# Kernel optimization log

Measured on AMD Instinct MI355X. Metric: run time of the kernel, lower is better.

Reference implementation:

```python
import jax, jax.numpy as jnp
import numpy as np
import math

D_MODEL = 2048
N_HEADS = 16
D_HEAD = D_MODEL // N_HEADS
SCALE = 1.0 / math.sqrt(D_HEAD)


def setup_inputs() -> dict:
    key = jax.random.key(0)
    kx, kq, kk, kv, ko = jax.random.split(key, 5)
    x = jax.random.normal(kx, (2, 2048, D_MODEL), dtype=jnp.float32)
    W_q = jax.random.normal(kq, (D_MODEL, D_MODEL), dtype=jnp.float32)
    W_k = jax.random.normal(kk, (D_MODEL, D_MODEL), dtype=jnp.float32)
    W_v = jax.random.normal(kv, (D_MODEL, D_MODEL), dtype=jnp.float32) * math.sqrt(2.0 / D_MODEL)
    W_o = jax.random.normal(ko, (D_MODEL, D_MODEL), dtype=jnp.float32) * math.sqrt(2.0 / D_MODEL)
    return {"x": x, "W_q": W_q, "W_k": W_k, "W_v": W_v, "W_o": W_o}


def reference(x, W_q, W_k, W_v, W_o) -> jnp.ndarray:
    B, S, D = x.shape
    q = (x @ W_q).reshape(B, S, N_HEADS, D_HEAD)  # [b, q, h, dh]
    k = (x @ W_k).reshape(B, S, N_HEADS, D_HEAD)  # [b, k, h, dh]
    v = x @ W_v                                    # [b, k, d_model] (NOT split into heads)
    scores = jnp.einsum('bqhd,bkhd->bhqk', q, k)   # [b, h, q, k]
    # Faithful quirk: additive -1e9 causal mask applied BEFORE the scale.
    mask = jnp.triu(jnp.full((S, S), -1e9, dtype=scores.dtype), k=1)
    scores = (scores + mask) * SCALE
    probs = jax.nn.softmax(scores, axis=-1)
    # Faithful quirk: sums over heads h AND keys k against full-width v.
    out = jnp.einsum('bhqk,bkd->bqd', probs, v)    # [b, q, d_model]
    return out @ W_o
```

## Files before the change

### kernel.cpp

```cpp
#include <hip/hip_runtime.h>

typedef unsigned short u16;
typedef __attribute__((ext_vector_type(8))) short bf16x8;
typedef __attribute__((ext_vector_type(4))) float f32x4;

#define DEV __device__ __forceinline__
#define EXP2(x) __builtin_amdgcn_exp2f(x)
#define LOG2(x) __builtin_amdgcn_logf(x)

DEV u16 f2bf(float f) {
  union { float f; unsigned u; } v; v.f = f;
  unsigned r = v.u + 0x7fffu + ((v.u >> 16) & 1u);
  return (u16)(r >> 16);
}
DEV float bf2f(u16 h) {
  union { unsigned u; float f; } v; v.u = ((unsigned)h) << 16;
  return v.f;
}
DEV f32x4 mfma16(bf16x8 a, bf16x8 b, f32x4 c) {
  return __builtin_amdgcn_mfma_f32_16x16x32_bf16(a, b, c, 0, 0, 0);
}
DEV void cp16(const u16* g, u16* l) {
  __builtin_amdgcn_global_load_lds((__attribute__((address_space(1))) void*)g,
                                   (__attribute__((address_space(3))) void*)l, 16, 0, 0);
}

__global__ __launch_bounds__(256) void split_pair(const float4* __restrict__ x,
                                                  u16* __restrict__ hi, u16* __restrict__ lo) {
  const size_t i = (size_t)blockIdx.x * 256 + threadIdx.x;
  const float4 v = x[i];
  ushort4 h, l;
  h.x = f2bf(v.x); l.x = f2bf(v.x - bf2f(h.x));
  h.y = f2bf(v.y); l.y = f2bf(v.y - bf2f(h.y));
  h.z = f2bf(v.z); l.z = f2bf(v.z - bf2f(h.z));
  h.w = f2bf(v.w); l.w = f2bf(v.w - bf2f(h.w));
  *(ushort4*)&hi[i * 4] = h;
  *(ushort4*)&lo[i * 4] = l;
}

template<bool LO>
__global__ __launch_bounds__(256) void transpose_split(const float* __restrict__ W,
                                                       u16* __restrict__ Th, u16* __restrict__ Tl) {
  __shared__ float t[64][65];
  const int r0 = blockIdx.y * 64, c0 = blockIdx.x * 64;
  const int rr = threadIdx.x >> 4, c4 = (threadIdx.x & 15) * 4;
#pragma unroll
  for (int p = 0; p < 4; ++p) {
    const float4 v = *(const float4*)&W[(size_t)(r0 + p * 16 + rr) * 2048 + c0 + c4];
    t[p * 16 + rr][c4 + 0] = v.x; t[p * 16 + rr][c4 + 1] = v.y;
    t[p * 16 + rr][c4 + 2] = v.z; t[p * 16 + rr][c4 + 3] = v.w;
  }
  __syncthreads();
#pragma unroll
  for (int p = 0; p < 4; ++p) {
    const int cc = p * 16 + rr;
    const float v0 = t[c4 + 0][cc], v1 = t[c4 + 1][cc], v2 = t[c4 + 2][cc], v3 = t[c4 + 3][cc];
    ushort4 h;
    h.x = f2bf(v0); h.y = f2bf(v1); h.z = f2bf(v2); h.w = f2bf(v3);
    *(ushort4*)&Th[(size_t)(c0 + cc) * 2048 + r0 + c4] = h;
    if constexpr (LO) {
      ushort4 l;
      l.x = f2bf(v0 - bf2f(h.x)); l.y = f2bf(v1 - bf2f(h.y));
      l.z = f2bf(v2 - bf2f(h.z)); l.w = f2bf(v3 - bf2f(h.w));
      *(ushort4*)&Tl[(size_t)(c0 + cc) * 2048 + r0 + c4] = l;
    }
  }
}

__global__ __launch_bounds__(256, 2) void gemm_qk(
    const u16* __restrict__ Aph, const u16* __restrict__ Apl,
    const u16* __restrict__ Bqh, const u16* __restrict__ Bql,
    const u16* __restrict__ Bkh, const u16* __restrict__ Bkl,
    u16* __restrict__ Qh, u16* __restrict__ Ql,
    u16* __restrict__ Kh, u16* __restrict__ Kl) {
  extern __shared__ u16 lds[];
  char* ldsb = (char*)lds;
  const int tid = threadIdx.x;
  const int wave = tid >> 6, lane = tid & 63;
  const int li = lane & 15, l4 = lane >> 4;
  const int lin0 = ((int)blockIdx.y << 4) | (int)blockIdx.x;
  const int xcd = lin0 & 7, idx = lin0 >> 3;
  const int m0 = ((xcd << 2) | (idx & 3)) * 128;
  const int n0 = (idx >> 2) * 128;
  const int wr = (wave >> 1) * 64, wc = (wave & 1) * 64;

  const f32x4 fz = {0.f, 0.f, 0.f, 0.f};
  f32x4 accQ[4][4], accK[4][4];
#pragma unroll
  for (int m = 0; m < 4; ++m)
#pragma unroll
    for (int n = 0; n < 4; ++n) { accQ[m][n] = fz; accK[m][n] = fz; }

  const int o = tid * 16;
  const int op = o ^ (((o >> 7) & 7) << 4);
  const int srow = op >> 6, scol = (op & 63) >> 1;
  const size_t aoff = (size_t)(m0 + srow) * 2048 + scol;
  const size_t boff = (size_t)(n0 + srow) * 2048 + scol;
  const size_t rstep = (size_t)64 * 2048;
  const int s0 = tid * 8, s1 = 2048 + tid * 8;

  const int arow = wr + li, brow = wc + li;
  const int rsA = (arow * 64 + l4 * 16) ^ (((arow >> 1) & 7) << 4);
  const int rsB = (brow * 64 + l4 * 16) ^ (((brow >> 1) & 7) << 4);

#pragma unroll 1
  for (int k0 = 0; k0 < 2048; k0 += 32) {
    cp16(Aph + aoff + k0,         &lds[s0]);
    cp16(Aph + aoff + rstep + k0, &lds[s1]);
    cp16(Apl + aoff + k0,         &lds[4096 + s0]);
    cp16(Apl + aoff + rstep + k0, &lds[4096 + s1]);
    cp16(Bqh + boff + k0,         &lds[8192 + s0]);
    cp16(Bqh + boff + rstep + k0, &lds[8192 + s1]);
    cp16(Bql + boff + k0,         &lds[12288 + s0]);
    cp16(Bql + boff + rstep + k0, &lds[12288 + s1]);
    cp16(Bkh + boff + k0,         &lds[16384 + s0]);
    cp16(Bkh + boff + rstep + k0, &lds[16384 + s1]);
    cp16(Bkl + boff + k0,         &lds[20480 + s0]);
    cp16(Bkl + boff + rstep + k0, &lds[20480 + s1]);
    __syncthreads();
    bf16x8 af[4], alf[4];
#pragma unroll
    for (int m = 0; m < 4; ++m) {
      af[m]  = *(const bf16x8*)(ldsb + rsA + m * 1024);
      alf[m] = *(const bf16x8*)(ldsb + 8192 + rsA + m * 1024);
    }
    {
      bf16x8 bh[4], bl[4];
#pragma unroll
      for (int n = 0; n < 4; ++n) {
        bh[n] = *(const bf16x8*)(ldsb + 16384 + rsB + n * 1024);
        bl[n] = *(const bf16x8*)(ldsb + 24576 + rsB + n * 1024);
      }
#pragma unroll
      for (int m = 0; m < 4; ++m)
#pragma unroll
        for (int n = 0; n < 4; ++n) {
          accQ[m][n] = mfma16(af[m], bh[n], accQ[m][n]);
          accQ[m][n] = mfma16(af[m], bl[n], accQ[m][n]);
          accQ[m][n] = mfma16(alf[m], bh[n], accQ[m][n]);
        }
    }
    {
      bf16x8 bh[4], bl[4];
#pragma unroll
      for (int n = 0; n < 4; ++n) {
        bh[n] = *(const bf16x8*)(ldsb + 32768 + rsB + n * 1024);
        bl[n] = *(const bf16x8*)(ldsb + 40960 + rsB + n * 1024);
      }
#pragma unroll
      for (int m = 0; m < 4; ++m)
#pragma unroll
        for (int n = 0; n < 4; ++n) {
          accK[m][n] = mfma16(af[m], bh[n], accK[m][n]);
          accK[m][n] = mfma16(af[m], bl[n], accK[m][n]);
          accK[m][n] = mfma16(alf[m], bh[n], accK[m][n]);
        }
    }
    __syncthreads();
  }

#pragma unroll
  for (int m = 0; m < 4; ++m) {
#pragma unroll
    for (int n = 0; n < 4; ++n) {
      const int rg0 = m0 + wr + m * 16 + l4 * 4;
      const int cg  = n0 + wc + n * 16 + li;
#pragma unroll
      for (int r = 0; r < 4; ++r) {
        const float vq = accQ[m][n][r];
        const u16 hq = f2bf(vq);
        Qh[(size_t)(rg0 + r) * 2048 + cg] = hq;
        Ql[(size_t)(rg0 + r) * 2048 + cg] = f2bf(vq - bf2f(hq));
        const float vk = accK[m][n][r];
        const u16 hk = f2bf(vk);
        Kh[(size_t)(rg0 + r) * 2048 + cg] = hk;
        Kl[(size_t)(rg0 + r) * 2048 + cg] = f2bf(vk - bf2f(hk));
      }
    }
  }
}

template<int OUTMODE, bool KLIM>
__global__ __launch_bounds__(256, 2) void gemm_bt(
    const u16* __restrict__ Aph, const u16* __restrict__ Bph,
    void* __restrict__ C0,
    const int M, const int N, const int K, const int bShift) {
  extern __shared__ u16 lds[];
  constexpr int T_BH = 4096;
  const int tid = threadIdx.x;
  const int wave = tid >> 6, lane = tid & 63;
  const int li = lane & 15, l4 = lane >> 4;
  const int lin0 = ((int)blockIdx.y << 4) | (int)blockIdx.x;
  const int xcd = lin0 & 7, idx = lin0 >> 3;
  const int m0 = ((xcd << 2) | (idx & 3)) * 128;
  const int n0 = (idx >> 2) * 128;
  const int wr = (wave >> 1) * 64, wc = (wave & 1) * 64;
  const u16* Bh = Bph;
  if (bShift) { const size_t s = (size_t)(m0 >> 11) * (size_t)bShift; Bh += s; }

  const f32x4 fz = {0.f, 0.f, 0.f, 0.f};
  f32x4 acc[4][4];
#pragma unroll
  for (int m = 0; m < 4; ++m)
#pragma unroll
    for (int n = 0; n < 4; ++n) acc[m][n] = fz;

  const size_t aoff = (size_t)(m0 + (tid >> 2)) * K + (tid & 3) * 8;
  const size_t boff = (size_t)(n0 + (tid >> 2)) * K + (tid & 3) * 8;
  const size_t rstep = (size_t)64 * K;
  const int s0 = tid * 8, s1 = 2048 + tid * 8;
  const int abase = (wr + li) * 32 + l4 * 8;
  const int bbase = (wc + li) * 32 + l4 * 8;
  const int kEnd = KLIM ? ((m0 & 2047) + 128 < K ? (m0 & 2047) + 128 : K) : K;

#pragma unroll 1
  for (int k0 = 0; k0 < kEnd; k0 += 32) {
    cp16(Aph + aoff + k0,         &lds[s0]);
    cp16(Aph + aoff + rstep + k0, &lds[s1]);
    cp16(Bh + boff + k0,          &lds[T_BH + s0]);
    cp16(Bh + boff + rstep + k0,  &lds[T_BH + s1]);
    __syncthreads();
    bf16x8 af[4], bf_[4];
#pragma unroll
    for (int m = 0; m < 4; ++m) af[m] = *(const bf16x8*)&lds[abase + m * 512];
#pragma unroll
    for (int n = 0; n < 4; ++n) bf_[n] = *(const bf16x8*)&lds[T_BH + bbase + n * 512];
#pragma unroll
    for (int m = 0; m < 4; ++m)
#pragma unroll
      for (int n = 0; n < 4; ++n)
        acc[m][n] = mfma16(af[m], bf_[n], acc[m][n]);
    __syncthreads();
  }

#pragma unroll
  for (int m = 0; m < 4; ++m) {
#pragma unroll
    for (int n = 0; n < 4; ++n) {
      const int rg0 = m0 + wr + m * 16 + l4 * 4;
      const int cg  = n0 + wc + n * 16 + li;
      if constexpr (OUTMODE == 1) {
        u16* Cs = (u16*)C0;
#pragma unroll
        for (int r = 0; r < 4; ++r) Cs[(size_t)(rg0 + r) * N + cg] = f2bf(acc[m][n][r]);
      } else if constexpr (OUTMODE == 2) {
        u16* Vt = (u16*)C0;
        ushort4 pk;
        pk.x = f2bf(acc[m][n][0]); pk.y = f2bf(acc[m][n][1]);
        pk.z = f2bf(acc[m][n][2]); pk.w = f2bf(acc[m][n][3]);
        *(ushort4*)&Vt[(size_t)(rg0 >> 11) * 4194304 + (size_t)cg * 2048 + (rg0 & 2047)] = pk;
      } else {
        float* Cf = (float*)C0;
#pragma unroll
        for (int r = 0; r < 4; ++r) Cf[(size_t)(rg0 + r) * N + cg] = acc[m][n][r];
      }
    }
  }
}

#define C2EXP 0.1275174381027786f

__global__ __launch_bounds__(256) void attn_lse_part(
    const u16* __restrict__ Qh, const u16* __restrict__ Ql,
    const u16* __restrict__ Kh, const u16* __restrict__ Kl,
    float* __restrict__ Mp, float* __restrict__ Lp) {
  const int j = blockIdx.x, qt = 15 - (int)blockIdx.y, hb = blockIdx.z;
  const int b = hb >> 4, h = hb & 15;
  const int tid = threadIdx.x;
  const int nch = (qt >> 2) + 1;
  if (j >= nch) {
    if (tid < 128) {
      const size_t o = ((size_t)hb * 4 + j) * 2048 + qt * 128 + tid;
      Mp[o] = -3.0e38f; Lp[o] = 0.f;
    }
    return;
  }
  __shared__ __align__(16) u16 kb[16384];
  const int wave = tid >> 6, lane = tid & 63;
  const int li = lane & 15, l4 = lane >> 4;
  const int q0w = qt * 128 + wave * 32;
  const int rs = ((li << 6) | (l4 << 4)) ^ (((li >> 1) & 7) << 4);

  bf16x8 qfh[2][4], qfl[2][4];
#pragma unroll
  for (int mf = 0; mf < 2; ++mf) {
    const size_t qo = ((size_t)(b * 2048 + q0w + mf * 16 + li)) * 2048 + h * 128 + l4 * 8;
#pragma unroll
    for (int ks = 0; ks < 4; ++ks) {
      qfh[mf][ks] = *(const bf16x8*)&Qh[qo + ks * 32];
      qfl[mf][ks] = *(const bf16x8*)&Ql[qo + ks * 32];
    }
  }
  float m[2][4], l[2][4];
#pragma unroll
  for (int mf = 0; mf < 2; ++mf)
#pragma unroll
    for (int r = 0; r < 4; ++r) { m[mf][r] = -3.0e38f; l[mf][r] = 0.f; }

  const int kst = j * 8;
  const int ken = min(j * 8 + 8, qt * 2 + 2);
  const size_t kgbase = ((size_t)b * 2048) * 2048 + h * 128;
  const f32x4 fz = {0.f, 0.f, 0.f, 0.f};

#pragma unroll 1
  for (int t = kst; t < ken; ++t) {
    __syncthreads();
#pragma unroll
    for (int i = 0; i < 4; ++i) {
      const int o = (tid + i * 256) * 16;
      const int op = o ^ (((o >> 7) & 7) << 4);
      const int dck = op >> 12, s = (op >> 6) & 63, dl = (op >> 1) & 31;
      const size_t g = kgbase + (size_t)(t * 64 + s) * 2048 + dck * 32 + dl;
      cp16(Kh + g, kb + (o >> 1));
      cp16(Kl + g, kb + 8192 + (o >> 1));
    }
    __syncthreads();
#pragma unroll
    for (int sn = 0; sn < 4; ++sn) {
      if (64 * t + 16 * sn <= q0w + 31) {
        f32x4 a0 = fz, a1 = fz;
        __builtin_amdgcn_s_setprio(1);
#pragma unroll
        for (int ks = 0; ks < 4; ++ks) {
          const bf16x8 kh = *(const bf16x8*)((const char*)kb + ks * 4096 + (sn << 10) + rs);
          const bf16x8 kl = *(const bf16x8*)((const char*)kb + 16384 + ks * 4096 + (sn << 10) + rs);
          a0 = mfma16(qfh[0][ks], kh, a0);
          a0 = mfma16(qfh[0][ks], kl, a0);
          a0 = mfma16(qfl[0][ks], kh, a0);
          a1 = mfma16(qfh[1][ks], kh, a1);
          a1 = mfma16(qfh[1][ks], kl, a1);
          a1 = mfma16(qfl[1][ks], kh, a1);
        }
        __builtin_amdgcn_s_setprio(0);
        const int kg = t * 64 + sn * 16 + li;
#pragma unroll
        for (int r = 0; r < 4; ++r) {
          {
            const float aa = (kg <= q0w + l4 * 4 + r) ? a0[r] : -3.3e38f;
            if (__all(aa <= m[0][r])) {
              l[0][r] += EXP2((aa - m[0][r]) * C2EXP);
            } else {
              const float mn = fmaxf(m[0][r], aa);
              l[0][r] = l[0][r] * EXP2((m[0][r] - mn) * C2EXP) + EXP2((aa - mn) * C2EXP);
              m[0][r] = mn;
            }
          }
          {
            const float aa = (kg <= q0w + 16 + l4 * 4 + r) ? a1[r] : -3.3e38f;
            if (__all(aa <= m[1][r])) {
              l[1][r] += EXP2((aa - m[1][r]) * C2EXP);
            } else {
              const float mn = fmaxf(m[1][r], aa);
              l[1][r] = l[1][r] * EXP2((m[1][r] - mn) * C2EXP) + EXP2((aa - mn) * C2EXP);
              m[1][r] = mn;
            }
          }
        }
      }
    }
  }
#pragma unroll
  for (int off = 1; off <= 8; off <<= 1) {
#pragma unroll
    for (int mf = 0; mf < 2; ++mf)
#pragma unroll
      for (int r = 0; r < 4; ++r) {
        const float om = __shfl_xor(m[mf][r], off, 64);
        const float ol = __shfl_xor(l[mf][r], off, 64);
        const float mn = fmaxf(m[mf][r], om);
        l[mf][r] = l[mf][r] * EXP2((m[mf][r] - mn) * C2EXP) + ol * EXP2((om - mn) * C2EXP);
        m[mf][r] = mn;
      }
  }
  if (li == 0) {
#pragma unroll
    for (int mf = 0; mf < 2; ++mf)
#pragma unroll
      for (int r = 0; r < 4; ++r) {
        const size_t o = ((size_t)hb * 4 + j) * 2048 + q0w + mf * 16 + l4 * 4 + r;
        Mp[o] = m[mf][r];
        Lp[o] = l[mf][r];
      }
  }
}

__global__ __launch_bounds__(256) void attn_lse_merge(
    const float* __restrict__ Mp, const float* __restrict__ Lp, float* __restrict__ LSE) {
  const int id = blockIdx.x * 256 + threadIdx.x;
  const int q = id & 2047, hb = id >> 11;
  const size_t base = (size_t)hb * 4 * 2048 + q;
  float m = Mp[base], l = Lp[base];
#pragma unroll
  for (int jj = 1; jj < 4; ++jj) {
    const float om = Mp[base + jj * 2048];
    const float ol = Lp[base + jj * 2048];
    const float mn = fmaxf(m, om);
    l = l * EXP2((m - mn) * C2EXP) + ol * EXP2((om - mn) * C2EXP);
    m = mn;
  }
  LSE[(size_t)hb * 2048 + q] = m * C2EXP + LOG2(l);
}

__global__ __launch_bounds__(256) void attn_psum(
    const u16* __restrict__ Qh, const u16* __restrict__ Ql,
    const u16* __restrict__ Kh, const u16* __restrict__ Kl,
    const float* __restrict__ LSE, u16* __restrict__ Psum) {
  const int kt = blockIdx.x, qt = blockIdx.y, b = blockIdx.z;
  const int q0 = qt * 128, k0 = kt * 128;
  const int tid = threadIdx.x;

  if (kt > qt) {
    const size_t o = ((size_t)(b * 2048 + q0 + (tid >> 1))) * 2048 + k0 + (tid & 1) * 64;
    const uint4 z = {0u, 0u, 0u, 0u};
#pragma unroll
    for (int j2 = 0; j2 < 8; ++j2) *(uint4*)&Psum[o + j2 * 8] = z;
    return;
  }

  extern __shared__ u16 kb2[];
  const int wave = tid >> 6, lane = tid & 63;
  const int li = lane & 15, l4 = lane >> 4;
  const int q0w = q0 + wave * 32;
  const int rs = ((li << 6) | (l4 << 4)) ^ (((li >> 1) & 7) << 4);
  const int snmax = (kt == qt) ? (wave * 2 + 2) : 8;

  const f32x4 fz = {0.f, 0.f, 0.f, 0.f};
  f32x4 ps[2][8];
#pragma unroll
  for (int mf = 0; mf < 2; ++mf)
#pragma unroll
    for (int sn = 0; sn < 8; ++sn) ps[mf][sn] = fz;

  const size_t kgbase = ((size_t)(b * 2048 + k0)) * 2048;
  const size_t qbase0 = ((size_t)(b * 2048 + q0w + li)) * 2048 + l4 * 8;
  const size_t qbase1 = qbase0 + (size_t)16 * 2048;
  const size_t lbase  = (size_t)(b * 16) * 2048 + q0w + l4 * 4;

#pragma unroll 1
  for (int h = 0; h < 16; ++h) {
    __syncthreads();
#pragma unroll
    for (int i = 0; i < 8; ++i) {
      const int o = (tid + i * 256) * 16;
      const int op = o ^ (((o >> 7) & 7) << 4);
      const int dck = op >> 13, s = (op >> 6) & 127, dl = (op >> 1) & 31;
      const size_t g = kgbase + (size_t)s * 2048 + h * 128 + dck * 32 + dl;
      cp16(Kh + g, kb2 + (o >> 1));
      cp16(Kl + g, kb2 + 16384 + (o >> 1));
    }
    bf16x8 qfh0[4], qfl0[4], qfh1[4], qfl1[4];
    float clse[2][4];
#pragma unroll
    for (int ks = 0; ks < 4; ++ks) {
      qfh0[ks] = *(const bf16x8*)&Qh[qbase0 + (size_t)h * 128 + ks * 32];
      qfl0[ks] = *(const bf16x8*)&Ql[qbase0 + (size_t)h * 128 + ks * 32];
      qfh1[ks] = *(const bf16x8*)&Qh[qbase1 + (size_t)h * 128 + ks * 32];
      qfl1[ks] = *(const bf16x8*)&Ql[qbase1 + (size_t)h * 128 + ks * 32];
    }
#pragma unroll
    for (int mf = 0; mf < 2; ++mf)
#pragma unroll
      for (int r = 0; r < 4; ++r)
        clse[mf][r] = LSE[lbase + (size_t)h * 2048 + mf * 16 + r];
    __syncthreads();

#pragma unroll
    for (int sn = 0; sn < 8; ++sn) {
      if (sn < snmax) {
        f32x4 a0 = fz, a1 = fz;
        __builtin_amdgcn_s_setprio(1);
#pragma unroll
        for (int ks = 0; ks < 4; ++ks) {
          const bf16x8 kh = *(const bf16x8*)((const char*)kb2 + ks * 8192 + (sn << 10) + rs);
          const bf16x8 kl = *(const bf16x8*)((const char*)kb2 + 32768 + ks * 8192 + (sn << 10) + rs);
          a0 = mfma16(qfh0[ks], kh, a0);
          a0 = mfma16(qfh0[ks], kl, a0);
          a0 = mfma16(qfl0[ks], kh, a0);
          a1 = mfma16(qfh1[ks], kh, a1);
          a1 = mfma16(qfh1[ks], kl, a1);
          a1 = mfma16(qfl1[ks], kh, a1);
        }
        __builtin_amdgcn_s_setprio(0);
        const int kg = k0 + sn * 16 + li;
#pragma unroll
        for (int r = 0; r < 4; ++r) {
          if (kg <= q0w + l4 * 4 + r)      ps[0][sn][r] += EXP2(a0[r] * C2EXP - clse[0][r]);
          if (kg <= q0w + 16 + l4 * 4 + r) ps[1][sn][r] += EXP2(a1[r] * C2EXP - clse[1][r]);
        }
      }
    }
  }

#pragma unroll
  for (int mf = 0; mf < 2; ++mf)
#pragma unroll
    for (int sn = 0; sn < 8; ++sn) {
      const size_t o0 = ((size_t)(b * 2048 + q0w + mf * 16 + l4 * 4)) * 2048 + k0 + sn * 16 + li;
#pragma unroll
      for (int r = 0; r < 4; ++r) Psum[o0 + (size_t)r * 2048] = f2bf(ps[mf][sn][r]);
    }
}

extern "C" void kernel_launch(void* const* d_in, const int* in_sizes, int n_in,
                              void* d_out, int out_size, void* d_ws, size_t ws_size,
                              hipStream_t stream) {
  (void)in_sizes; (void)n_in; (void)out_size; (void)ws_size;
  const float* x  = (const float*)d_in[0];
  const float* Wq = (const float*)d_in[1];
  const float* Wk = (const float*)d_in[2];
  const float* Wv = (const float*)d_in[3];
  const float* Wo = (const float*)d_in[4];
  u16* ws = (u16*)d_ws;
  const size_t E8 = 8388608, E4 = 4194304;
  u16* xh = ws;
  u16* xl = ws + E8;
  u16* Qh = ws + 2 * E8;
  u16* Ql = ws + 3 * E8;
  u16* Kh = ws + 4 * E8;
  u16* Kl = ws + 5 * E8;
  u16* Vt = ws + 6 * E8;
  u16* WTh = ws + 7 * E8;
  u16* WTl = ws + 7 * E8 + E4;
  u16* WTb = ws + 7 * E8 + 2 * E4;
  u16* WkTh = Vt;
  u16* WkTl = Vt + E4;
  float* LSEf = (float*)WTl;
  float* Mp   = LSEf + 65536;
  float* Lp   = Mp + 262144;
  u16* Psum = xl;
  u16* out1 = xh;

  split_pair<<<8192, 256, 0, stream>>>((const float4*)x, xh, xl);

  dim3 tg(32, 32);

  transpose_split<true ><<<tg, 256, 0, stream>>>(Wq, WTh, WTl);
  transpose_split<true ><<<tg, 256, 0, stream>>>(Wk, WkTh, WkTl);
  transpose_split<false><<<tg, 256, 0, stream>>>(Wv, WTb, nullptr);

  gemm_qk<<<dim3(16, 32), 256, 49152, stream>>>(
      xh, xl, WTh, WTl, WkTh, WkTl, Qh, Ql, Kh, Kl);

  gemm_bt<2, false><<<dim3(16, 32), 256, 16384, stream>>>(
      xh, WTb, Vt, 4096, 2048, 2048, 0);

  attn_lse_part<<<dim3(4, 16, 32), 256, 0, stream>>>(Qh, Ql, Kh, Kl, Mp, Lp);
  attn_lse_merge<<<256, 256, 0, stream>>>(Mp, Lp, LSEf);
  attn_psum<<<dim3(16, 16, 2), 256, 65536, stream>>>(Qh, Ql, Kh, Kl, LSEf, Psum);

  gemm_bt<1, true><<<dim3(16, 32), 256, 16384, stream>>>(
      Psum, Vt, out1, 4096, 2048, 2048, 4194304);

  transpose_split<false><<<tg, 256, 0, stream>>>(Wo, WTb, nullptr);
  gemm_bt<3, false><<<dim3(16, 32), 256, 16384, stream>>>(
      out1, WTb, d_out, 4096, 2048, 2048, 0);
}
```

Baseline: 565.5 us.

## Halve attn_psum key tile, split MFMA accumulators, merge weight transposes

Shrinks the attn_psum key tile from 128 to 64, doubling the grid. It uses 32KB of static LDS instead of 64KB dynamic, to raise occupancy and trim causal waste on the diagonal. The hi/lo compensated MFMA chain now uses independent accumulators to break the serial dependency. The three weight transposes are fused into one launch to cut launch overhead. In exchange, Q fragments and LSE values are reloaded twice as often across key tiles.

Result: slower. 616.0 us (+8.9%).

```diff
diff --git a/kernel.cpp b/kernel.cpp
--- a/kernel.cpp
+++ b/kernel.cpp
@@ -36,6 +36,40 @@
   h.w = f2bf(v.w); l.w = f2bf(v.w - bf2f(h.w));
   *(ushort4*)&hi[i * 4] = h;
   *(ushort4*)&lo[i * 4] = l;
+}
+
+__global__ __launch_bounds__(256) void transpose_all(
+    const float* __restrict__ Wq, const float* __restrict__ Wk, const float* __restrict__ Wv,
+    u16* __restrict__ qTh, u16* __restrict__ qTl,
+    u16* __restrict__ kTh, u16* __restrict__ kTl, u16* __restrict__ vTh) {
+  const float* W; u16* Th; u16* Tl; bool LO;
+  if (blockIdx.z == 0)      { W = Wq; Th = qTh; Tl = qTl;     LO = true;  }
+  else if (blockIdx.z == 1) { W = Wk; Th = kTh; Tl = kTl;     LO = true;  }
+  else                      { W = Wv; Th = vTh; Tl = nullptr; LO = false; }
+  __shared__ float t[64][65];
+  const int r0 = blockIdx.y * 64, c0 = blockIdx.x * 64;
+  const int rr = threadIdx.x >> 4, c4 = (threadIdx.x & 15) * 4;
+#pragma unroll
+  for (int p = 0; p < 4; ++p) {
+    const float4 v = *(const float4*)&W[(size_t)(r0 + p * 16 + rr) * 2048 + c0 + c4];
+    t[p * 16 + rr][c4 + 0] = v.x; t[p * 16 + rr][c4 + 1] = v.y;
+    t[p * 16 + rr][c4 + 2] = v.z; t[p * 16 + rr][c4 + 3] = v.w;
+  }
+  __syncthreads();
+#pragma unroll
+  for (int p = 0; p < 4; ++p) {
+    const int cc = p * 16 + rr;
+    const float v0 = t[c4 + 0][cc], v1 = t[c4 + 1][cc], v2 = t[c4 + 2][cc], v3 = t[c4 + 3][cc];
+    ushort4 h;
+    h.x = f2bf(v0); h.y = f2bf(v1); h.z = f2bf(v2); h.w = f2bf(v3);
+    *(ushort4*)&Th[(size_t)(c0 + cc) * 2048 + r0 + c4] = h;
+    if (LO) {
+      ushort4 l;
+      l.x = f2bf(v0 - bf2f(h.x)); l.y = f2bf(v1 - bf2f(h.y));
+      l.z = f2bf(v2 - bf2f(h.z)); l.w = f2bf(v3 - bf2f(h.w));
+      *(ushort4*)&Tl[(size_t)(c0 + cc) * 2048 + r0 + c4] = l;
+    }
+  }
 }
 
 template<bool LO>
@@ -406,30 +440,31 @@
     const u16* __restrict__ Kh, const u16* __restrict__ Kl,
     const float* __restrict__ LSE, u16* __restrict__ Psum) {
   const int kt = blockIdx.x, qt = blockIdx.y, b = blockIdx.z;
-  const int q0 = qt * 128, k0 = kt * 128;
+  const int q0 = qt * 128, k0 = kt * 64;
   const int tid = threadIdx.x;
 
-  if (kt > qt) {
-    const size_t o = ((size_t)(b * 2048 + q0 + (tid >> 1))) * 2048 + k0 + (tid & 1) * 64;
+  if (k0 > q0 + 127) {
+    const size_t o = ((size_t)(b * 2048 + q0 + (tid >> 1))) * 2048 + k0 + (tid & 1) * 32;
     const uint4 z = {0u, 0u, 0u, 0u};
 #pragma unroll
-    for (int j2 = 0; j2 < 8; ++j2) *(uint4*)&Psum[o + j2 * 8] = z;
+    for (int j2 = 0; j2 < 4; ++j2) *(uint4*)&Psum[o + j2 * 8] = z;
     return;
   }
 
-  extern __shared__ u16 kb2[];
+  __shared__ __align__(16) u16 kb[16384];
   const int wave = tid >> 6, lane = tid & 63;
   const int li = lane & 15, l4 = lane >> 4;
   const int q0w = q0 + wave * 32;
   const int rs = ((li << 6) | (l4 << 4)) ^ (((li >> 1) & 7) << 4);
-  const int snmax = (kt == qt) ? (wave * 2 + 2) : 8;
+  int snmax = ((q0w + 31 - k0) >> 4) + 1;
+  snmax = snmax < 0 ? 0 : (snmax > 4 ? 4 : snmax);
 
   const f32x4 fz = {0.f, 0.f, 0.f, 0.f};
-  f32x4 ps[2][8];
+  f32x4 ps[2][4];
 #pragma unroll
   for (int mf = 0; mf < 2; ++mf)
 #pragma unroll
-    for (int sn = 0; sn < 8; ++sn) ps[mf][sn] = fz;
+    for (int sn = 0; sn < 4; ++sn) ps[mf][sn] = fz;
 
   const size_t kgbase = ((size_t)(b * 2048 + k0)) * 2048;
   const size_t qbase0 = ((size_t)(b * 2048 + q0w + li)) * 2048 + l4 * 8;
@@ -440,13 +475,13 @@
   for (int h = 0; h < 16; ++h) {
     __syncthreads();
 #pragma unroll
-    for (int i = 0; i < 8; ++i) {
+    for (int i = 0; i < 4; ++i) {
       const int o = (tid + i * 256) * 16;
       const int op = o ^ (((o >> 7) & 7) << 4);
-      const int dck = op >> 13, s = (op >> 6) & 127, dl = (op >> 1) & 31;
+      const int dck = op >> 12, s = (op >> 6) & 63, dl = (op >> 1) & 31;
       const size_t g = kgbase + (size_t)s * 2048 + h * 128 + dck * 32 + dl;
-      cp16(Kh + g, kb2 + (o >> 1));
-      cp16(Kl + g, kb2 + 16384 + (o >> 1));
+      cp16(Kh + g, kb + (o >> 1));
+      cp16(Kl + g, kb + 8192 + (o >> 1));
     }
     bf16x8 qfh0[4], qfl0[4], qfh1[4], qfl1[4];
     float clse[2][4];
@@ -465,22 +500,24 @@
     __syncthreads();
 
 #pragma unroll
-    for (int sn = 0; sn < 8; ++sn) {
+    for (int sn = 0; sn < 4; ++sn) {
       if (sn < snmax) {
-        f32x4 a0 = fz, a1 = fz;
+        f32x4 aA = fz, aB = fz, aC = fz, bA = fz, bB = fz, bC = fz;
         __builtin_amdgcn_s_setprio(1);
 #pragma unroll
         for (int ks = 0; ks < 4; ++ks) {
-          const bf16x8 kh = *(const bf16x8*)((const char*)kb2 + ks * 8192 + (sn << 10) + rs);
-          const bf16x8 kl = *(const bf16x8*)((const char*)kb2 + 32768 + ks * 8192 + (sn << 10) + rs);
-          a0 = mfma16(qfh0[ks], kh, a0);
-          a0 = mfma16(qfh0[ks], kl, a0);
-          a0 = mfma16(qfl0[ks], kh, a0);
-          a1 = mfma16(qfh1[ks], kh, a1);
-          a1 = mfma16(qfh1[ks], kl, a1);
-          a1 = mfma16(qfl1[ks], kh, a1);
+          const bf16x8 kh = *(const bf16x8*)((const char*)kb + ks * 4096 + (sn << 10) + rs);
+          const bf16x8 kl = *(const bf16x8*)((const char*)kb + 16384 + ks * 4096 + (sn << 10) + rs);
+          aA = mfma16(qfh0[ks], kh, aA);
+          aB = mfma16(qfh0[ks], kl, aB);
+          aC = mfma16(qfl0[ks], kh, aC);
+          bA = mfma16(qfh1[ks], kh, bA);
+          bB = mfma16(qfh1[ks], kl, bB);
+          bC = mfma16(qfl1[ks], kh, bC);
         }
         __builtin_amdgcn_s_setprio(0);
+        const f32x4 a0 = (aA + aB) + aC;
+        const f32x4 a1 = (bA + bB) + bC;
         const int kg = k0 + sn * 16 + li;
 #pragma unroll
         for (int r = 0; r < 4; ++r) {
@@ -494,7 +531,7 @@
 #pragma unroll
   for (int mf = 0; mf < 2; ++mf)
 #pragma unroll
-    for (int sn = 0; sn < 8; ++sn) {
+    for (int sn = 0; sn < 4; ++sn) {
       const size_t o0 = ((size_t)(b * 2048 + q0w + mf * 16 + l4 * 4)) * 2048 + k0 + sn * 16 + li;
 #pragma unroll
       for (int r = 0; r < 4; ++r) Psum[o0 + (size_t)r * 2048] = f2bf(ps[mf][sn][r]);
@@ -532,11 +569,8 @@
 
   split_pair<<<8192, 256, 0, stream>>>((const float4*)x, xh, xl);
 
-  dim3 tg(32, 32);
-
-  transpose_split<true ><<<tg, 256, 0, stream>>>(Wq, WTh, WTl);
-  transpose_split<true ><<<tg, 256, 0, stream>>>(Wk, WkTh, WkTl);
-  transpose_split<false><<<tg, 256, 0, stream>>>(Wv, WTb, nullptr);
+  transpose_all<<<dim3(32, 32, 3), 256, 0, stream>>>(
+      Wq, Wk, Wv, WTh, WTl, WkTh, WkTl, WTb);
 
   gemm_qk<<<dim3(16, 32), 256, 49152, stream>>>(
       xh, xl, WTh, WTl, WkTh, WkTl, Qh, Ql, Kh, Kl);
@@ -546,12 +580,12 @@
 
   attn_lse_part<<<dim3(4, 16, 32), 256, 0, stream>>>(Qh, Ql, Kh, Kl, Mp, Lp);
   attn_lse_merge<<<256, 256, 0, stream>>>(Mp, Lp, LSEf);
-  attn_psum<<<dim3(16, 16, 2), 256, 65536, stream>>>(Qh, Ql, Kh, Kl, LSEf, Psum);
+  attn_psum<<<dim3(32, 16, 2), 256, 0, stream>>>(Qh, Ql, Kh, Kl, LSEf, Psum);
 
   gemm_bt<1, true><<<dim3(16, 32), 256, 16384, stream>>>(
       Psum, Vt, out1, 4096, 2048, 2048, 4194304);
 
-  transpose_split<false><<<tg, 256, 0, stream>>>(Wo, WTb, nullptr);
+  transpose_split<false><<<dim3(32, 32), 256, 0, stream>>>(Wo, WTb, nullptr);
   gemm_bt<3, false><<<dim3(16, 32), 256, 16384, stream>>>(
       out1, WTb, d_out, 4096, 2048, 2048, 0);
 }
```

## Fuse V projection into QK GEMM and batch weight transposes into one launch

Applied to the files above, without the earlier changes.

Adds a gemm_qkv kernel that computes the Q, K and V projections in one pass. Each x tile loaded into LDS is reused for all three outputs, and the V result is written directly in the transposed layout. The three separate weight transpose/split launches become one 3D-grid launch. This is meant to remove a second full read of x, one GEMM launch and two transpose launches. In exchange it needs extra workspace for the K weights, falls back to the old path if the workspace is too small, and holds three accumulator sets per wave, which raises register pressure.

Measured after the change: 600.6 us. 1.06x slower.

```diff
diff --git a/kernel.cpp b/kernel.cpp
--- a/kernel.cpp
+++ b/kernel.cpp
@@ -38,6 +38,40 @@
   *(ushort4*)&lo[i * 4] = l;
 }
 
+__global__ __launch_bounds__(256) void transpose_all(
+    const float* __restrict__ Wq, const float* __restrict__ Wk, const float* __restrict__ Wv,
+    u16* __restrict__ qTh, u16* __restrict__ qTl,
+    u16* __restrict__ kTh, u16* __restrict__ kTl, u16* __restrict__ vTh) {
+  const float* W; u16* Th; u16* Tl; bool LO;
+  if (blockIdx.z == 0)      { W = Wq; Th = qTh; Tl = qTl;     LO = true;  }
+  else if (blockIdx.z == 1) { W = Wk; Th = kTh; Tl = kTl;     LO = true;  }
+  else                      { W = Wv; Th = vTh; Tl = nullptr; LO = false; }
+  __shared__ float t[64][65];
+  const int r0 = blockIdx.y * 64, c0 = blockIdx.x * 64;
+  const int rr = threadIdx.x >> 4, c4 = (threadIdx.x & 15) * 4;
+#pragma unroll
+  for (int p = 0; p < 4; ++p) {
+    const float4 v = *(const float4*)&W[(size_t)(r0 + p * 16 + rr) * 2048 + c0 + c4];
+    t[p * 16 + rr][c4 + 0] = v.x; t[p * 16 + rr][c4 + 1] = v.y;
+    t[p * 16 + rr][c4 + 2] = v.z; t[p * 16 + rr][c4 + 3] = v.w;
+  }
+  __syncthreads();
+#pragma unroll
+  for (int p = 0; p < 4; ++p) {
+    const int cc = p * 16 + rr;
+    const float v0 = t[c4 + 0][cc], v1 = t[c4 + 1][cc], v2 = t[c4 + 2][cc], v3 = t[c4 + 3][cc];
+    ushort4 h;
+    h.x = f2bf(v0); h.y = f2bf(v1); h.z = f2bf(v2); h.w = f2bf(v3);
+    *(ushort4*)&Th[(size_t)(c0 + cc) * 2048 + r0 + c4] = h;
+    if (LO) {
+      ushort4 l;
+      l.x = f2bf(v0 - bf2f(h.x)); l.y = f2bf(v1 - bf2f(h.y));
+      l.z = f2bf(v2 - bf2f(h.z)); l.w = f2bf(v3 - bf2f(h.w));
+      *(ushort4*)&Tl[(size_t)(c0 + cc) * 2048 + r0 + c4] = l;
+    }
+  }
+}
+
 template<bool LO>
 __global__ __launch_bounds__(256) void transpose_split(const float* __restrict__ W,
                                                        u16* __restrict__ Th, u16* __restrict__ Tl) {
@@ -63,6 +97,129 @@
       l.x = f2bf(v0 - bf2f(h.x)); l.y = f2bf(v1 - bf2f(h.y));
       l.z = f2bf(v2 - bf2f(h.z)); l.w = f2bf(v3 - bf2f(h.w));
       *(ushort4*)&Tl[(size_t)(c0 + cc) * 2048 + r0 + c4] = l;
+    }
+  }
+}
+
+__global__ __launch_bounds__(512, 2) void gemm_qkv(
+    const u16* __restrict__ Aph, const u16* __restrict__ Apl,
+    const u16* __restrict__ Bqh, const u16* __restrict__ Bql,
+    const u16* __restrict__ Bkh, const u16* __restrict__ Bkl,
+    const u16* __restrict__ Bvh,
+    u16* __restrict__ Qh, u16* __restrict__ Ql,
+    u16* __restrict__ Kh, u16* __restrict__ Kl, u16* __restrict__ Vt) {
+  extern __shared__ u16 lds[];
+  char* ldsb = (char*)lds;
+  const int tid = threadIdx.x;
+  const int wave = tid >> 6, lane = tid & 63;
+  const int li = lane & 15, l4 = lane >> 4;
+  const int lin0 = ((int)blockIdx.y << 4) | (int)blockIdx.x;
+  const int xcd = lin0 & 7, idx = lin0 >> 3;
+  const int m0 = ((xcd << 2) | (idx & 3)) * 128;
+  const int n0 = (idx >> 2) * 128;
+  const int wr = (wave >> 1) * 32, wc = (wave & 1) * 64;
+
+  const f32x4 fz = {0.f, 0.f, 0.f, 0.f};
+  f32x4 aQ[2][4], aK[2][4], aV[2][4];
+#pragma unroll
+  for (int mm = 0; mm < 2; ++mm)
+#pragma unroll
+    for (int nn = 0; nn < 4; ++nn) { aQ[mm][nn] = fz; aK[mm][nn] = fz; aV[mm][nn] = fz; }
+
+  const int o = tid * 16;
+  const int op = o ^ (((o >> 7) & 7) << 4);
+  const int srow = op >> 6, scol = (op & 63) >> 1;
+  const size_t aoff = (size_t)(m0 + srow) * 2048 + scol;
+  const size_t boff = (size_t)(n0 + srow) * 2048 + scol;
+  const int sd = o >> 1;
+
+  const int arow = wr + li, brow = wc + li;
+  const int rsA = (arow * 64 + l4 * 16) ^ (((arow >> 1) & 7) << 4);
+  const int rsB = (brow * 64 + l4 * 16) ^ (((brow >> 1) & 7) << 4);
+
+#pragma unroll 1
+  for (int k0 = 0; k0 < 2048; k0 += 32) {
+    cp16(Aph + aoff + k0, &lds[sd]);
+    cp16(Apl + aoff + k0, &lds[4096 + sd]);
+    cp16(Bqh + boff + k0, &lds[8192 + sd]);
+    cp16(Bql + boff + k0, &lds[12288 + sd]);
+    cp16(Bkh + boff + k0, &lds[16384 + sd]);
+    cp16(Bkl + boff + k0, &lds[20480 + sd]);
+    cp16(Bvh + boff + k0, &lds[24576 + sd]);
+    __syncthreads();
+    bf16x8 af[2], alf[2];
+#pragma unroll
+    for (int mm = 0; mm < 2; ++mm) {
+      af[mm]  = *(const bf16x8*)(ldsb + rsA + mm * 1024);
+      alf[mm] = *(const bf16x8*)(ldsb + 8192 + rsA + mm * 1024);
+    }
+    {
+      bf16x8 bh[4], bl[4];
+#pragma unroll
+      for (int nn = 0; nn < 4; ++nn) {
+        bh[nn] = *(const bf16x8*)(ldsb + 16384 + rsB + nn * 1024);
+        bl[nn] = *(const bf16x8*)(ldsb + 24576 + rsB + nn * 1024);
+      }
+#pragma unroll
+      for (int mm = 0; mm < 2; ++mm)
+#pragma unroll
+        for (int nn = 0; nn < 4; ++nn) {
+          aQ[mm][nn] = mfma16(af[mm], bh[nn], aQ[mm][nn]);
+          aQ[mm][nn] = mfma16(af[mm], bl[nn], aQ[mm][nn]);
+          aQ[mm][nn] = mfma16(alf[mm], bh[nn], aQ[mm][nn]);
+        }
+    }
+    {
+      bf16x8 bh[4], bl[4];
+#pragma unroll
+      for (int nn = 0; nn < 4; ++nn) {
+        bh[nn] = *(const bf16x8*)(ldsb + 32768 + rsB + nn * 1024);
+        bl[nn] = *(const bf16x8*)(ldsb + 40960 + rsB + nn * 1024);
+      }
+#pragma unroll
+      for (int mm = 0; mm < 2; ++mm)
+#pragma unroll
+        for (int nn = 0; nn < 4; ++nn) {
+          aK[mm][nn] = mfma16(af[mm], bh[nn], aK[mm][nn]);
+          aK[mm][nn] = mfma16(af[mm], bl[nn], aK[mm][nn]);
+          aK[mm][nn] = mfma16(alf[mm], bh[nn], aK[mm][nn]);
+        }
+    }
+    {
+      bf16x8 bh[4];
+#pragma unroll
+      for (int nn = 0; nn < 4; ++nn)
+        bh[nn] = *(const bf16x8*)(ldsb + 49152 + rsB + nn * 1024);
+#pragma unroll
+      for (int mm = 0; mm < 2; ++mm)
+#pragma unroll
+        for (int nn = 0; nn < 4; ++nn)
+          aV[mm][nn] = mfma16(af[mm], bh[nn], aV[mm][nn]);
+    }
+    __syncthreads();
+  }
+
+#pragma unroll
+  for (int mm = 0; mm < 2; ++mm) {
+#pragma unroll
+    for (int nn = 0; nn < 4; ++nn) {
+      const int rg0 = m0 + wr + mm * 16 + l4 * 4;
+      const int cg  = n0 + wc + nn * 16 + li;
+#pragma unroll
+      for (int r = 0; r < 4; ++r) {
+        const float vq = aQ[mm][nn][r];
+        const u16 hq = f2bf(vq);
+        Qh[(size_t)(rg0 + r) * 2048 + cg] = hq;
+        Ql[(size_t)(rg0 + r) * 2048 + cg] = f2bf(vq - bf2f(hq));
+        const float vk = aK[mm][nn][r];
+        const u16 hk = f2bf(vk);
+        Kh[(size_t)(rg0 + r) * 2048 + cg] = hk;
+        Kl[(size_t)(rg0 + r) * 2048 + cg] = f2bf(vk - bf2f(hk));
+      }
+      ushort4 pk;
+      pk.x = f2bf(aV[mm][nn][0]); pk.y = f2bf(aV[mm][nn][1]);
+      pk.z = f2bf(aV[mm][nn][2]); pk.w = f2bf(aV[mm][nn][3]);
+      *(ushort4*)&Vt[(size_t)(rg0 >> 11) * 4194304 + (size_t)cg * 2048 + (rg0 & 2047)] = pk;
     }
   }
 }
@@ -504,7 +661,7 @@
 extern "C" void kernel_launch(void* const* d_in, const int* in_sizes, int n_in,
                               void* d_out, int out_size, void* d_ws, size_t ws_size,
                               hipStream_t stream) {
-  (void)in_sizes; (void)n_in; (void)out_size; (void)ws_size;
+  (void)in_sizes; (void)n_in; (void)out_size;
   const float* x  = (const float*)d_in[0];
   const float* Wq = (const float*)d_in[1];
   const float* Wk = (const float*)d_in[2];
@@ -522,27 +679,31 @@
   u16* WTh = ws + 7 * E8;
   u16* WTl = ws + 7 * E8 + E4;
   u16* WTb = ws + 7 * E8 + 2 * E4;
-  u16* WkTh = Vt;
-  u16* WkTl = Vt + E4;
   float* LSEf = (float*)WTl;
   float* Mp   = LSEf + 65536;
   float* Lp   = Mp + 262144;
   u16* Psum = xl;
   u16* out1 = xh;
 
+  const size_t need_qkv = (7 * E8 + 5 * E4) * sizeof(u16);
+  const bool use_qkv = (ws_size >= need_qkv);
+  u16* WkTh = use_qkv ? (ws + 7 * E8 + 3 * E4) : Vt;
+  u16* WkTl = use_qkv ? (ws + 7 * E8 + 4 * E4) : (Vt + E4);
+
   split_pair<<<8192, 256, 0, stream>>>((const float4*)x, xh, xl);
 
-  dim3 tg(32, 32);
-
-  transpose_split<true ><<<tg, 256, 0, stream>>>(Wq, WTh, WTl);
-  transpose_split<true ><<<tg, 256, 0, stream>>>(Wk, WkTh, WkTl);
-  transpose_split<false><<<tg, 256, 0, stream>>>(Wv, WTb, nullptr);
-
-  gemm_qk<<<dim3(16, 32), 256, 49152, stream>>>(
-      xh, xl, WTh, WTl, WkTh, WkTl, Qh, Ql, Kh, Kl);
-
-  gemm_bt<2, false><<<dim3(16, 32), 256, 16384, stream>>>(
-      xh, WTb, Vt, 4096, 2048, 2048, 0);
+  transpose_all<<<dim3(32, 32, 3), 256, 0, stream>>>(
+      Wq, Wk, Wv, WTh, WTl, WkTh, WkTl, WTb);
+
+  if (use_qkv) {
+    gemm_qkv<<<dim3(16, 32), 512, 57344, stream>>>(
+        xh, xl, WTh, WTl, WkTh, WkTl, WTb, Qh, Ql, Kh, Kl, Vt);
+  } else {
+    gemm_qk<<<dim3(16, 32), 256, 49152, stream>>>(
+        xh, xl, WTh, WTl, WkTh, WkTl, Qh, Ql, Kh, Kl);
+    gemm_bt<2, false><<<dim3(16, 32), 256, 16384, stream>>>(
+        xh, WTb, Vt, 4096, 2048, 2048, 0);
+  }
 
   attn_lse_part<<<dim3(4, 16, 32), 256, 0, stream>>>(Qh, Ql, Kh, Kl, Mp, Lp);
   attn_lse_merge<<<256, 256, 0, stream>>>(Mp, Lp, LSEf);
@@ -551,7 +712,7 @@
   gemm_bt<1, true><<<dim3(16, 32), 256, 16384, stream>>>(
       Psum, Vt, out1, 4096, 2048, 2048, 4194304);
 
-  transpose_split<false><<<tg, 256, 0, stream>>>(Wo, WTb, nullptr);
+  transpose_split<false><<<dim3(32, 32), 256, 0, stream>>>(Wo, WTb, nullptr);
   gemm_bt<3, false><<<dim3(16, 32), 256, 16384, stream>>>(
       out1, WTb, d_out, 4096, 2048, 2048, 0);
 }
```
